# Performance work log

Measured on AMD Instinct MI355X. Metric: run time of the kernel, lower is better.

## Reference

```python
import jax, jax.numpy as jnp
import numpy as np

N, D_IN, D_ATTN = 8192, 48, 8


def setup_inputs() -> dict:
    key = jax.random.key(0)
    ks = jax.random.split(key, 9)
    s = 1.0 / np.sqrt(D_IN)
    return {
        "x": jax.random.normal(ks[0], (N, D_IN), jnp.float32),
        "Kw": jax.random.normal(ks[1], (D_IN, D_ATTN), jnp.float32) * s,
        "Kb": jax.random.normal(ks[2], (D_ATTN,), jnp.float32) * s,
        "Qw": jax.random.normal(ks[3], (D_IN, D_ATTN), jnp.float32) * s,
        "Qb": jax.random.normal(ks[4], (D_ATTN,), jnp.float32) * s,
        "Vw": jax.random.normal(ks[5], (D_IN, D_ATTN), jnp.float32) * s,
        "Vb": jax.random.normal(ks[6], (D_ATTN,), jnp.float32) * s,
        "Zw": jax.random.normal(ks[7], (D_ATTN, D_IN), jnp.float32) * (1.0 / np.sqrt(D_ATTN)),
        "Zb": jax.random.normal(ks[8], (D_IN,), jnp.float32) * (1.0 / np.sqrt(D_ATTN)),
    }


def reference(x, Kw, Kb, Qw, Qb, Vw, Vb, Zw, Zb):
    # Tiny QKV projections: [N,48] -> [N,8]
    Xk = x @ Kw + Kb
    Xq = x @ Qw + Qb
    Xv = x @ Vw + Vb
    # Attention over the batch/row dimension: [N,8]@[8,N] -> [N,N]
    scale = jnp.sqrt(jnp.asarray(D_ATTN, jnp.float32))
    AM = jax.nn.softmax(Xk @ Xq.T / scale, axis=1)  # torch F.softmax 2D default dim=1
    Z = AM @ Xv                                      # [N,8]
    return x + (Z @ Zw + Zb)                         # residual + output proj [N,48]
```

## Files before the change

### kernel.cpp

```cpp
#include <hip/hip_runtime.h>
#include <hip/hip_fp16.h>


#define QV_OFF   32768
#define BMAX_OFF 98304
#define PART_OFF 98560

typedef _Float16 hv2 __attribute__((ext_vector_type(2)));
union HVU { unsigned u; hv2 v; };

static __device__ __forceinline__ unsigned pku(float a, float b) {
    auto t = __builtin_amdgcn_cvt_pkrtz(a, b);
    union { decltype(t) x; unsigned u; } c; c.x = t; return c.u;
}
static __device__ __forceinline__ hv2 asV(unsigned u) { HVU t; t.u = u; return t.v; }
static __device__ __forceinline__ hv2 h2fma(hv2 a, hv2 b, hv2 c) {
#if __has_builtin(__builtin_elementwise_fma)
    return __builtin_elementwise_fma(a, b, c);
#else
    union { hv2 v; __half2 h; } A, B, C, D;
    A.v = a; B.v = b; C.v = c;
    D.h = __hfma2(A.h, B.h, C.h);
    return D.v;
#endif
}
static __device__ __forceinline__ unsigned dupL(unsigned u) {
    const unsigned lo = u & 0xFFFFu; return lo | (lo << 16);
}
static __device__ __forceinline__ unsigned dupH(unsigned u) {
    const unsigned hi = u >> 16; return hi | (hi << 16);
}

__global__ __launch_bounds__(256) void proj_kernel(
    const float* __restrict__ x,
    const float* __restrict__ Kw, const float* __restrict__ Kb,
    const float* __restrict__ Qw, const float* __restrict__ Qb,
    const float* __restrict__ Vw, const float* __restrict__ Vb,
    unsigned* __restrict__ Xksf16, unsigned* __restrict__ QV,
    float* __restrict__ bmax)
{
    __shared__ float xs[32 * 49];
    __shared__ float wAll[3 * 388];
    __shared__ float bs[24];
    __shared__ float outv[32][25];
    const int tid = threadIdx.x;
    const int r0 = blockIdx.x * 32;

    for (int i = tid; i < 1536; i += 256) {
        int r = i / 48, c = i - r * 48;
        xs[r * 49 + c] = x[r0 * 48 + i];
    }
    for (int i = tid; i < 384; i += 256) {
        wAll[i]       = Kw[i];
        wAll[388 + i] = Qw[i];
        wAll[776 + i] = Vw[i];
    }
    if (tid < 8)       bs[tid] = Kb[tid];
    else if (tid < 16) bs[tid] = Qb[tid - 8];
    else if (tid < 24) bs[tid] = Vb[tid - 16];
    __syncthreads();

    const int rl = tid >> 3;
    const int g  = tid & 7;
    const int c0 = 3 * g;
    const float* xr = &xs[rl * 49];
    const float* w0 = &wAll[((c0 + 0) >> 3) * 388 + ((c0 + 0) & 7)];
    const float* w1 = &wAll[((c0 + 1) >> 3) * 388 + ((c0 + 1) & 7)];
    const float* w2 = &wAll[((c0 + 2) >> 3) * 388 + ((c0 + 2) & 7)];
    float a0 = bs[c0], a1 = bs[c0 + 1], a2 = bs[c0 + 2];
    #pragma unroll
    for (int k = 0; k < 48; k++) {
        const float xv = xr[k];
        a0 = fmaf(xv, w0[k * 8], a0);
        a1 = fmaf(xv, w1[k * 8], a1);
        a2 = fmaf(xv, w2[k * 8], a2);
    }
    outv[rl][c0] = a0; outv[rl][c0 + 1] = a1; outv[rl][c0 + 2] = a2;
    __syncthreads();

    {
        const int p = tid >> 4;
        const int c = (tid >> 1) & 7;
        const int m = tid & 1;
        const int col = (m ? 16 : 8) + c;
        QV[(blockIdx.x * 16 + p) * 16 + m * 8 + c] =
            pku(outv[2 * p][col], outv[2 * p + 1][col]);
    }
    const float kscale = 0.51008732149f;
    if (tid < 32) {
        uint4 o;
        o.x = pku(outv[tid][0] * kscale, outv[tid][1] * kscale);
        o.y = pku(outv[tid][2] * kscale, outv[tid][3] * kscale);
        o.z = pku(outv[tid][4] * kscale, outv[tid][5] * kscale);
        o.w = pku(outv[tid][6] * kscale, outv[tid][7] * kscale);
        ((uint4*)Xksf16)[r0 + tid] = o;
    }
    if (tid >= 192 && tid < 224) {
        const int r = tid - 192;
        float n2 = 0.f;
        #pragma unroll
        for (int c = 0; c < 8; c++) n2 = fmaf(outv[r][8 + c], outv[r][8 + c], n2);
        #pragma unroll
        for (int off = 16; off > 0; off >>= 1)
            n2 = fmaxf(n2, __shfl_xor(n2, off, 64));
        if (r == 0) bmax[blockIdx.x] = n2;
    }
}

__global__ __launch_bounds__(256, 4) void attn_kernel(
    const unsigned* __restrict__ Xksf16, const unsigned* __restrict__ QV,
    const float* __restrict__ bmax,
    float* __restrict__ part, int ppw)
{
    __shared__ uint4 sh4[2304];
    uint4* slab = sh4;
    float* redf = (float*)sh4;

    const int tid  = threadIdx.x;
    const int lane = tid & 63;
    const int wv   = tid >> 6;
    const int rgrp  = blockIdx.x & 31;
    const int chunk = blockIdx.x >> 5;

    float m = fmaxf(fmaxf(bmax[lane], bmax[64 + lane]),
                    fmaxf(bmax[128 + lane], bmax[192 + lane]));
    #pragma unroll
    for (int off = 32; off > 0; off >>= 1)
        m = fmaxf(m, __shfl_xor(m, off, 64));
    const float qmax2 = m;

    unsigned kd[4][8];
    hv2 sinit2[4], l2[4], acc[4][8];
    const hv2 one2 = asV(0x3C003C00u);
    #pragma unroll
    for (int i = 0; i < 4; ++i) {
        const uint4 kv = ((const uint4*)Xksf16)[rgrp * 256 + i * 64 + lane];
        kd[i][0] = dupL(kv.x); kd[i][1] = dupH(kv.x);
        kd[i][2] = dupL(kv.y); kd[i][3] = dupH(kv.y);
        kd[i][4] = dupL(kv.z); kd[i][5] = dupH(kv.z);
        kd[i][6] = dupL(kv.w); kd[i][7] = dupH(kv.w);
        float kn2 = 0.f;
        #pragma unroll
        for (int c = 0; c < 8; c++) {
            const float kf = (float)asV(kd[i][c]).x;
            kn2 = fmaf(kf, kf, kn2);
        }
        const float sinit = -sqrtf(kn2 * qmax2);
        sinit2[i] = asV(pku(sinit, sinit));
        l2[i] = asV(0u);
        #pragma unroll
        for (int c = 0; c < 8; c++) acc[i][c] = asV(0u);
    }

    const uint4* QV4 = (const uint4*)QV;
    const int nt = ppw >> 5;

    for (int t = 0; t < nt; ++t) {
        for (int i = tid; i < 512; i += 256) {
            const int w = i >> 7;
            const int j = i & 127;
            slab[i] = QV4[(size_t)((((chunk * 4 + w) * ppw + (t << 5)) << 2) + j)];
        }
        __syncthreads();

        const uint4* sw = &slab[wv << 7];
        #pragma unroll 2
        for (int p = 0; p < 32; ++p) {
            const uint4 qp0 = sw[p * 4 + 0];
            const uint4 qp1 = sw[p * 4 + 1];
            const uint4 vp0 = sw[p * 4 + 2];
            const uint4 vp1 = sw[p * 4 + 3];
            #pragma unroll
            for (int i = 0; i < 4; ++i) {
                hv2 s2 = sinit2[i];
                s2 = h2fma(asV(kd[i][0]), asV(qp0.x), s2);
                s2 = h2fma(asV(kd[i][1]), asV(qp0.y), s2);
                s2 = h2fma(asV(kd[i][2]), asV(qp0.z), s2);
                s2 = h2fma(asV(kd[i][3]), asV(qp0.w), s2);
                s2 = h2fma(asV(kd[i][4]), asV(qp1.x), s2);
                s2 = h2fma(asV(kd[i][5]), asV(qp1.y), s2);
                s2 = h2fma(asV(kd[i][6]), asV(qp1.z), s2);
                s2 = h2fma(asV(kd[i][7]), asV(qp1.w), s2);
                const float pa = __builtin_amdgcn_exp2f((float)s2.x);
                const float pb = __builtin_amdgcn_exp2f((float)s2.y);
                const hv2 ph = asV(pku(pa, pb));
                l2[i] = h2fma(ph, one2, l2[i]);
                acc[i][0] = h2fma(ph, asV(vp0.x), acc[i][0]);
                acc[i][1] = h2fma(ph, asV(vp0.y), acc[i][1]);
                acc[i][2] = h2fma(ph, asV(vp0.z), acc[i][2]);
                acc[i][3] = h2fma(ph, asV(vp0.w), acc[i][3]);
                acc[i][4] = h2fma(ph, asV(vp1.x), acc[i][4]);
                acc[i][5] = h2fma(ph, asV(vp1.y), acc[i][5]);
                acc[i][6] = h2fma(ph, asV(vp1.z), acc[i][6]);
                acc[i][7] = h2fma(ph, asV(vp1.w), acc[i][7]);
            }
        }
        __syncthreads();
    }

    #pragma unroll
    for (int i = 0; i < 4; ++i) {
        const int r = i * 64 + lane;
        #pragma unroll
        for (int c = 0; c < 8; c++)
            redf[(wv * 256 + r) * 9 + c] = (float)acc[i][c].x + (float)acc[i][c].y;
        redf[(wv * 256 + r) * 9 + 8] = (float)l2[i].x + (float)l2[i].y;
    }
    __syncthreads();
    for (int e = tid; e < 2304; e += 256) {
        const int r = e / 9, c = e - r * 9;
        const float s = redf[(0 * 256 + r) * 9 + c] + redf[(1 * 256 + r) * 9 + c]
                      + redf[(2 * 256 + r) * 9 + c] + redf[(3 * 256 + r) * 9 + c];
        part[((size_t)chunk * 8192 + rgrp * 256 + r) * 9 + c] = s;
    }
}

__global__ __launch_bounds__(256) void finish_kernel(
    const float* __restrict__ x,
    const float* __restrict__ Zw, const float* __restrict__ Zb,
    const float* __restrict__ part, float* __restrict__ out, int nch)
{
    __shared__ float Zs[32 * 9];
    __shared__ float Zl[32];
    __shared__ float zw_s[384];
    __shared__ float zb_s[48];
    const int tid = threadIdx.x;
    const int r0 = blockIdx.x * 32;

    for (int i = tid; i < 384; i += 256) zw_s[i] = Zw[i];
    if (tid < 48) zb_s[tid] = Zb[tid];

    {
        const int r = tid >> 3, c = tid & 7;
        float a = 0.f, l = 0.f;
        #pragma unroll 4
        for (int ch = 0; ch < nch; ch++) {
            const float* p = part + ((size_t)ch * 8192 + r0 + r) * 9;
            a += p[c];
            if (c == 0) l += p[8];
        }
        if (c == 0) Zl[r] = l;
        __syncthreads();
        Zs[r * 9 + c] = a * (1.0f / Zl[r]);
    }
    __syncthreads();

    for (int e = tid; e < 32 * 48; e += 256) {
        const int r = e / 48, c = e - r * 48;
        float o = x[r0 * 48 + e] + zb_s[c];
        #pragma unroll
        for (int k = 0; k < 8; k++) o = fmaf(Zs[r * 9 + k], zw_s[k * 48 + c], o);
        out[r0 * 48 + e] = o;
    }
}

extern "C" void kernel_launch(void* const* d_in, const int* in_sizes, int n_in,
                              void* d_out, int out_size, void* d_ws, size_t ws_size,
                              hipStream_t stream) {
    const float* x  = (const float*)d_in[0];
    const float* Kw = (const float*)d_in[1];
    const float* Kb = (const float*)d_in[2];
    const float* Qw = (const float*)d_in[3];
    const float* Qb = (const float*)d_in[4];
    const float* Vw = (const float*)d_in[5];
    const float* Vb = (const float*)d_in[6];
    const float* Zw = (const float*)d_in[7];
    const float* Zb = (const float*)d_in[8];
    float* out = (float*)d_out;

    float* ws = (float*)d_ws;
    unsigned* Xksf16 = (unsigned*)ws;
    unsigned* QV     = (unsigned*)(ws + QV_OFF);
    float* bmax      = ws + BMAX_OFF;
    float* part      = ws + PART_OFF;

    int nch = 32;
    const size_t avail = ws_size / 4;
    while (nch > 1 && (size_t)PART_OFF + (size_t)nch * 8192 * 9 > avail) nch >>= 1;
    const int ppw = 1024 / nch;

    proj_kernel<<<256, 256, 0, stream>>>(x, Kw, Kb, Qw, Qb, Vw, Vb,
                                         Xksf16, QV, bmax);
    attn_kernel<<<32 * nch, 256, 0, stream>>>(Xksf16, QV, bmax, part, ppw);
    finish_kernel<<<256, 256, 0, stream>>>(x, Zw, Zb, part, out, nch);
}
```

Baseline: 119.1 us.

## Broadcast Q/V tiles via readlane instead of LDS staging with barriers

```diff
diff --git a/kernel.cpp b/kernel.cpp
--- a/kernel.cpp
+++ b/kernel.cpp
@@ -107,14 +107,12 @@
     }
 }
 
-__global__ __launch_bounds__(256, 4) void attn_kernel(
+__global__ __launch_bounds__(256) void attn_kernel(
     const unsigned* __restrict__ Xksf16, const unsigned* __restrict__ QV,
     const float* __restrict__ bmax,
     float* __restrict__ part, int ppw)
 {
-    __shared__ uint4 sh4[2304];
-    uint4* slab = sh4;
-    float* redf = (float*)sh4;
+    __shared__ float redf[4 * 256 * 9];
 
     const int tid  = threadIdx.x;
     const int lane = tid & 63;
@@ -153,49 +151,60 @@
     }
 
     const uint4* QV4 = (const uint4*)QV;
-    const int nt = ppw >> 5;
-
-    for (int t = 0; t < nt; ++t) {
-        for (int i = tid; i < 512; i += 256) {
-            const int w = i >> 7;
-            const int j = i & 127;
-            slab[i] = QV4[(size_t)((((chunk * 4 + w) * ppw + (t << 5)) << 2) + j)];
-        }
-        __syncthreads();
-
-        const uint4* sw = &slab[wv << 7];
+    const int ntile = ppw >> 5;
+
+    for (int t = 0; t < ntile; ++t) {
+        const int pb = (chunk * 4 + wv) * ppw + t * 32 + (lane & 31);
+        const uint4* src = QV4 + (size_t)pb * 4;
+        const uint4 ta = src[0];
+        const uint4 tb = src[1];
+        const uint4 tc = src[2];
+        const uint4 td = src[3];
+
         #pragma unroll 2
         for (int p = 0; p < 32; ++p) {
-            const uint4 qp0 = sw[p * 4 + 0];
-            const uint4 qp1 = sw[p * 4 + 1];
-            const uint4 vp0 = sw[p * 4 + 2];
-            const uint4 vp1 = sw[p * 4 + 3];
+            unsigned qb[8], vb[8];
+            qb[0] = (unsigned)__builtin_amdgcn_readlane((int)ta.x, p);
+            qb[1] = (unsigned)__builtin_amdgcn_readlane((int)ta.y, p);
+            qb[2] = (unsigned)__builtin_amdgcn_readlane((int)ta.z, p);
+            qb[3] = (unsigned)__builtin_amdgcn_readlane((int)ta.w, p);
+            qb[4] = (unsigned)__builtin_amdgcn_readlane((int)tb.x, p);
+            qb[5] = (unsigned)__builtin_amdgcn_readlane((int)tb.y, p);
+            qb[6] = (unsigned)__builtin_amdgcn_readlane((int)tb.z, p);
+            qb[7] = (unsigned)__builtin_amdgcn_readlane((int)tb.w, p);
+            vb[0] = (unsigned)__builtin_amdgcn_readlane((int)tc.x, p);
+            vb[1] = (unsigned)__builtin_amdgcn_readlane((int)tc.y, p);
+            vb[2] = (unsigned)__builtin_amdgcn_readlane((int)tc.z, p);
+            vb[3] = (unsigned)__builtin_amdgcn_readlane((int)tc.w, p);
+            vb[4] = (unsigned)__builtin_amdgcn_readlane((int)td.x, p);
+            vb[5] = (unsigned)__builtin_amdgcn_readlane((int)td.y, p);
+            vb[6] = (unsigned)__builtin_amdgcn_readlane((int)td.z, p);
+            vb[7] = (unsigned)__builtin_amdgcn_readlane((int)td.w, p);
             #pragma unroll
             for (int i = 0; i < 4; ++i) {
                 hv2 s2 = sinit2[i];
-                s2 = h2fma(asV(kd[i][0]), asV(qp0.x), s2);
-                s2 = h2fma(asV(kd[i][1]), asV(qp0.y), s2);
-                s2 = h2fma(asV(kd[i][2]), asV(qp0.z), s2);
-                s2 = h2fma(asV(kd[i][3]), asV(qp0.w), s2);
-                s2 = h2fma(asV(kd[i][4]), asV(qp1.x), s2);
-                s2 = h2fma(asV(kd[i][5]), asV(qp1.y), s2);
-                s2 = h2fma(asV(kd[i][6]), asV(qp1.z), s2);
-                s2 = h2fma(asV(kd[i][7]), asV(qp1.w), s2);
-                const float pa = __builtin_amdgcn_exp2f((float)s2.x);
-                const float pb = __builtin_amdgcn_exp2f((float)s2.y);
-                const hv2 ph = asV(pku(pa, pb));
+                s2 = h2fma(asV(kd[i][0]), asV(qb[0]), s2);
+                s2 = h2fma(asV(kd[i][1]), asV(qb[1]), s2);
+                s2 = h2fma(asV(kd[i][2]), asV(qb[2]), s2);
+                s2 = h2fma(asV(kd[i][3]), asV(qb[3]), s2);
+                s2 = h2fma(asV(kd[i][4]), asV(qb[4]), s2);
+                s2 = h2fma(asV(kd[i][5]), asV(qb[5]), s2);
+                s2 = h2fma(asV(kd[i][6]), asV(qb[6]), s2);
+                s2 = h2fma(asV(kd[i][7]), asV(qb[7]), s2);
+                const float pa  = __builtin_amdgcn_exp2f((float)s2.x);
+                const float pbv = __builtin_amdgcn_exp2f((float)s2.y);
+                const hv2 ph = asV(pku(pa, pbv));
                 l2[i] = h2fma(ph, one2, l2[i]);
-                acc[i][0] = h2fma(ph, asV(vp0.x), acc[i][0]);
-                acc[i][1] = h2fma(ph, asV(vp0.y), acc[i][1]);
-                acc[i][2] = h2fma(ph, asV(vp0.z), acc[i][2]);
-                acc[i][3] = h2fma(ph, asV(vp0.w), acc[i][3]);
-                acc[i][4] = h2fma(ph, asV(vp1.x), acc[i][4]);
-                acc[i][5] = h2fma(ph, asV(vp1.y), acc[i][5]);
-                acc[i][6] = h2fma(ph, asV(vp1.z), acc[i][6]);
-                acc[i][7] = h2fma(ph, asV(vp1.w), acc[i][7]);
+                acc[i][0] = h2fma(ph, asV(vb[0]), acc[i][0]);
+                acc[i][1] = h2fma(ph, asV(vb[1]), acc[i][1]);
+                acc[i][2] = h2fma(ph, asV(vb[2]), acc[i][2]);
+                acc[i][3] = h2fma(ph, asV(vb[3]), acc[i][3]);
+                acc[i][4] = h2fma(ph, asV(vb[4]), acc[i][4]);
+                acc[i][5] = h2fma(ph, asV(vb[5]), acc[i][5]);
+                acc[i][6] = h2fma(ph, asV(vb[6]), acc[i][6]);
+                acc[i][7] = h2fma(ph, asV(vb[7]), acc[i][7]);
             }
         }
-        __syncthreads();
     }
 
     #pragma unroll
```

After: 123.9 us. +4.1%, slower.
